# Kernel optimization log

Measured on AMD Instinct MI355X. Metric: run time of the kernel, lower is better.

## Reference

```python
import jax, jax.numpy as jnp
import numpy as np

B, T, D = 8, 512, 1024
H, DQK, DV = 16, 128, 128  # n_heads, d_qk = emb_dim//h_qk, d_v = emb_dim//h_v


def setup_inputs() -> dict:
    key = jax.random.key(0)
    ks = jax.random.split(key, 8)
    s = 0.02
    return {
        "X": jax.random.normal(ks[0], (B, T, D), jnp.float32),
        "pos_enc_k": jax.random.normal(ks[1], (T, T, DQK), jnp.float32) * s,
        "pos_enc_v": jax.random.normal(ks[2], (T, T, DV), jnp.float32) * s,
        "Wq": jax.random.normal(ks[3], (D, H * DQK), jnp.float32) * s,
        "bq": jnp.zeros((H * DQK,), jnp.float32),
        "Wk": jax.random.normal(ks[4], (D, H * DQK), jnp.float32) * s,
        "bk": jnp.zeros((H * DQK,), jnp.float32),
        "Wv": jax.random.normal(ks[5], (D, H * DV), jnp.float32) * s,
        "bv": jnp.zeros((H * DV,), jnp.float32),
        "Wp": jax.random.normal(ks[6], (H * DV, D), jnp.float32) * s,
        "bp": jnp.zeros((D,), jnp.float32),
    }


def reference(X, pos_enc_k, pos_enc_v, Wq, bq, Wk, bk, Wv, bv, Wp, bp):
    b, t, d = X.shape
    # projections -> (b, h, t, dhead)
    Q = (X @ Wq + bq).reshape(b, t, H, DQK).transpose(0, 2, 1, 3)
    K = (X @ Wk + bk).reshape(b, t, H, DQK).transpose(0, 2, 1, 3)
    V = (X @ Wv + bv).reshape(b, t, H, DV).transpose(0, 2, 1, 3)
    # content attention + relative-position key bias
    att = jnp.einsum("bhqd,bhkd->bhqk", Q, K)
    att = att + jnp.einsum("bhqd,qkd->bhqk", Q, pos_enc_k)
    att = att / jnp.sqrt(jnp.asarray(DQK, X.dtype))
    # causal mask (do_mask=True)
    causal = jnp.tril(jnp.ones((t, t), bool))
    att = jnp.where(causal[None, None], att, jnp.asarray(-jnp.inf, att.dtype))
    att = jax.nn.softmax(att, axis=-1)
    # values + relative-position value correction
    y = jnp.einsum("bhqk,bhkd->bhqd", att, V)
    y = y + jnp.einsum("bhqk,qkd->bhqd", att, pos_enc_v)
    y = y.transpose(0, 2, 1, 3).reshape(b, t, H * DV)
    return y @ Wp + bp
```

## Files before the change

kernel.cpp:

```cpp
#include <hip/hip_runtime.h>
#include <stdint.h>

#define B_  8
#define T_  512
#define D_  1024
#define H_  16
#define DH  128
#define BH  128
#define ND  2048
#define BT  4096

typedef __attribute__((ext_vector_type(8))) short          short8;
typedef __attribute__((ext_vector_type(8))) __bf16         bf16x8;
typedef __attribute__((ext_vector_type(4))) float          f32x4;
typedef __attribute__((ext_vector_type(4))) unsigned short ushort4v;

static __device__ __forceinline__ unsigned short f2bf(float f) {
  unsigned u = __builtin_bit_cast(unsigned, f);
  u += 0x7FFFu + ((u >> 16) & 1u);
  return (unsigned short)(u >> 16);
}
static __device__ __forceinline__ float bf2f(unsigned short h) {
  unsigned u = ((unsigned)h) << 16;
  return __builtin_bit_cast(float, u);
}
static __device__ __forceinline__ f32x4 mfma16(short8 a, short8 b, f32x4 c) {
  return __builtin_amdgcn_mfma_f32_16x16x32_bf16(
      __builtin_bit_cast(bf16x8, a), __builtin_bit_cast(bf16x8, b), c, 0, 0, 0);
}
static __device__ __forceinline__ void gload16(const unsigned short* g, unsigned short* l) {
  __builtin_amdgcn_global_load_lds(
      (const __attribute__((address_space(1))) void*)g,
      (__attribute__((address_space(3))) void*)l, 16, 0, 0);
}

template <int ROWS, int COLS>
static __device__ __forceinline__ void stage_gl2(unsigned short* lds,
                                                 const unsigned short* __restrict__ src,
                                                 long stride, int tid) {
  constexpr int CPR = COLS / 8;
#pragma unroll
  for (int it = 0; it < ROWS * COLS / 8 / 256; ++it) {
    int chunk = tid + it * 256;
    int r = chunk / CPR, c8 = (chunk % CPR) * 8;
    gload16(src + (long)r * stride + c8, lds + chunk * 8);
  }
}

template <int ROWS>
static __device__ __forceinline__ void stage_sw64(unsigned short* lds,
                                                  const unsigned short* __restrict__ src,
                                                  long stride, int tid) {
#pragma unroll
  for (int it = 0; it < ROWS / 32; ++it) {
    int n = tid + it * 256;
    int r = n >> 3, c = (n & 7) ^ (r & 7);
    gload16(src + (long)r * stride + c * 8, lds + n * 8);
  }
}

template <int MR, int NR, int LDA, int LDB, int KD>
static __device__ __forceinline__ void mfma_blk(const unsigned short* As,
                                                const unsigned short* Bs,
                                                int a0, int b0, int lrow, int lk8,
                                                f32x4 (*acc)[NR]) {
#pragma unroll
  for (int ks = 0; ks < KD; ks += 32) {
    short8 a[MR], b[NR];
#pragma unroll
    for (int i = 0; i < MR; ++i) a[i] = *(const short8*)&As[(a0 + i * 16 + lrow) * LDA + ks + lk8];
#pragma unroll
    for (int j = 0; j < NR; ++j) b[j] = *(const short8*)&Bs[(b0 + j * 16 + lrow) * LDB + ks + lk8];
#pragma unroll
    for (int i = 0; i < MR; ++i)
#pragma unroll
      for (int j = 0; j < NR; ++j) acc[i][j] = mfma16(a[i], b[j], acc[i][j]);
  }
}

template <int MR, int NR>
static __device__ __forceinline__ void mfma_sw64(const unsigned short* As,
                                                 const unsigned short* Bs,
                                                 int a0, int b0, int lrow, int g,
                                                 f32x4 (*acc)[NR]) {
#pragma unroll
  for (int ks = 0; ks < 2; ++ks) {
    short8 a[MR], b[NR];
#pragma unroll
    for (int i = 0; i < MR; ++i) {
      int ra = a0 + i * 16 + lrow;
      int c = (ks * 4 + g) ^ (ra & 7);
      a[i] = *(const short8*)&As[ra * 64 + c * 8];
    }
#pragma unroll
    for (int j = 0; j < NR; ++j) {
      int rb = b0 + j * 16 + lrow;
      int c = (ks * 4 + g) ^ (rb & 7);
      b[j] = *(const short8*)&Bs[rb * 64 + c * 8];
    }
#pragma unroll
    for (int i = 0; i < MR; ++i)
#pragma unroll
      for (int j = 0; j < NR; ++j) acc[i][j] = mfma16(a[i], b[j], acc[i][j]);
  }
}

#define IDS4                             \
  const int tid  = threadIdx.x;          \
  const int lane = tid & 63;             \
  const int wid  = tid >> 6;             \
  const int lrow = lane & 15;            \
  const int lk8  = (lane >> 4) * 8;      \
  const int lr4  = (lane >> 4) * 4;      \
  const int lg   = lane >> 4;            \
  const int wm = wid >> 1, wn = wid & 1;

#define LTS 132
#define LTQ 68

__global__ __launch_bounds__(256) void k_prep(const float* __restrict__ X,
                                              unsigned short* __restrict__ Xb,
                                              const float* __restrict__ Wq,
                                              const float* __restrict__ Wk,
                                              const float* __restrict__ Wv,
                                              const float* __restrict__ Wp,
                                              unsigned short* __restrict__ WT,
                                              unsigned short* __restrict__ WpT) {
  __shared__ float tile[32][33];
  int bid = blockIdx.x;
  if (bid < 4096) {
    int i = bid * 256 + threadIdx.x;
    f32x4 v = ((const f32x4*)X)[i];
    ushort4v o;
    o.x = f2bf(v.x); o.y = f2bf(v.y); o.z = f2bf(v.z); o.w = f2bf(v.w);
    ((ushort4v*)Xb)[i] = o;
    return;
  }
  bid -= 4096;
  const int which = bid >> 11;
  const int local = bid & 2047;
  const float* in;
  unsigned short* outp;
  int R, C, bx, by;
  if (which < 3) {
    in = which == 0 ? Wq : (which == 1 ? Wk : Wv);
    outp = WT + (size_t)which * ND * D_;
    R = D_; C = ND; bx = local & 63; by = local >> 6;
  } else {
    in = Wp; outp = WpT;
    R = ND; C = D_; bx = local & 31; by = local >> 5;
  }
  int c0 = bx * 32, r0 = by * 32;
  int tx = threadIdx.x & 31, ty = threadIdx.x >> 5;
#pragma unroll
  for (int i = 0; i < 32; i += 8)
    tile[ty + i][tx] = in[(long)(r0 + ty + i) * C + (c0 + tx)];
  __syncthreads();
#pragma unroll
  for (int i = 0; i < 32; i += 8)
    outp[(long)(c0 + ty + i) * R + (r0 + tx)] = f2bf(tile[tx][ty + i]);
}

__global__ __launch_bounds__(256) void k_vtrans(const unsigned short* __restrict__ vin,
                                                unsigned short* __restrict__ vout) {
  __shared__ unsigned short tile[32][33];
  int bh = blockIdx.z;
  int t0 = blockIdx.x * 32, d0 = blockIdx.y * 32;
  int tx = threadIdx.x & 31, ty = threadIdx.x >> 5;
#pragma unroll
  for (int i = 0; i < 32; i += 8)
    tile[ty + i][tx] = vin[((long)bh * T_ + t0 + ty + i) * DH + (d0 + tx)];
  __syncthreads();
#pragma unroll
  for (int i = 0; i < 32; i += 8)
    vout[((long)bh * DH + (d0 + ty + i)) * T_ + (t0 + tx)] = tile[tx][ty + i];
}

__global__ __launch_bounds__(256) void k_proj8(const unsigned short* __restrict__ Xb,
                                               const unsigned short* __restrict__ WT,
                                               const float* __restrict__ bq,
                                               const float* __restrict__ bk,
                                               const float* __restrict__ bv,
                                               unsigned short* __restrict__ Qb,
                                               unsigned short* __restrict__ Kb,
                                               unsigned short* __restrict__ Vb) {
  __shared__ unsigned short As[128 * 64], Bs[128 * 64];
  IDS4
  const int flat = blockIdx.x, xcd = flat & 7, local = flat >> 3;
  const int nt = xcd * 6 + (local % 6);
  const int mt = local / 6;
  const int m0 = mt * 128, n0 = nt * 128;

  f32x4 acc[4][4] = {};
  for (int kk = 0; kk < D_; kk += 64) {
    stage_gl2<128, 64>(As, Xb + (long)m0 * D_ + kk, D_, tid);
    stage_gl2<128, 64>(Bs, WT + (long)n0 * D_ + kk, D_, tid);
    __syncthreads();
    mfma_blk<4, 4, 64, 64, 64>(As, Bs, wm * 64, wn * 64, lrow, lk8, acc);
    __syncthreads();
  }

  const int nb = n0 >> 11;
  const float* biasp = nb == 0 ? bq : (nb == 1 ? bk : bv);
  unsigned short* dst = nb == 0 ? Qb : (nb == 1 ? Kb : Vb);
  const int hcol = (n0 & 2047) >> 7;
#pragma unroll
  for (int i = 0; i < 4; ++i)
#pragma unroll
    for (int j = 0; j < 4; ++j) {
      int cc = (n0 & 2047) + wn * 64 + j * 16 + lrow;
      int dd = cc & 127;
      float bias = biasp[cc];
#pragma unroll
      for (int r = 0; r < 4; ++r) {
        int m = m0 + wm * 64 + i * 16 + lr4 + r;
        int bb = m >> 9, tt = m & (T_ - 1);
        dst[((long)(bb * H_ + hcol) * T_ + tt) * DH + dd] = f2bf(acc[i][j][r] + bias);
      }
    }
}

__global__ __launch_bounds__(256) void k_posk(const unsigned short* __restrict__ Qb,
                                              const float* __restrict__ Pk,
                                              unsigned short* __restrict__ att) {
  const int bid = blockIdx.x;
  const int q = (bid & 1) ? (T_ - 1 - (bid >> 1)) : (bid >> 1);
  const int ktiles = (q >> 6) + 1;
  __shared__ unsigned short As[128 * 128];
  __shared__ unsigned short Bs[2][64 * 136];
  IDS4
  {
    const unsigned short* src = Qb + (long)q * DH;
#pragma unroll
    for (int it = 0; it < 8; ++it) {
      int n = tid + it * 256;
      int r = n >> 4, c = (n & 15) ^ (r & 7);
      gload16(src + (long)r * (T_ * DH) + c * 8, As + n * 8);
    }
  }
  f32x4 pv[8];
  const float* psrc = Pk + (long)q * T_ * DH;
  auto loadPk = [&](int kt) {
#pragma unroll
    for (int it = 0; it < 8; ++it) {
      int chunk = tid + it * 256;
      int r = chunk >> 5, c4 = (chunk & 31) * 4;
      pv[it] = *(const f32x4*)(psrc + (long)(kt * 64 + r) * DH + c4);
    }
  };
  auto writeB = [&](int buf) {
#pragma unroll
    for (int it = 0; it < 8; ++it) {
      int chunk = tid + it * 256;
      int r = chunk >> 5, c4 = (chunk & 31) * 4;
      ushort4v o;
      o.x = f2bf(pv[it].x); o.y = f2bf(pv[it].y); o.z = f2bf(pv[it].z); o.w = f2bf(pv[it].w);
      *(ushort4v*)&Bs[buf][r * 136 + c4] = o;
    }
  };
  loadPk(0);
  asm volatile("s_waitcnt vmcnt(0)" ::: "memory");
  writeB(0);
  asm volatile("s_waitcnt lgkmcnt(0)" ::: "memory");
  __builtin_amdgcn_s_barrier();
  for (int kt = 0; kt < ktiles; ++kt) {
    const bool pre = (kt + 1 < ktiles);
    if (pre) loadPk(kt + 1);
    f32x4 acc[4][2] = {};
#pragma unroll
    for (int ks = 0; ks < 4; ++ks) {
      short8 a[4], b[2];
#pragma unroll
      for (int i = 0; i < 4; ++i) {
        int ra = wm * 64 + i * 16 + lrow;
        int c = (ks * 4 + lg) ^ (ra & 7);
        a[i] = *(const short8*)&As[ra * 128 + c * 8];
      }
#pragma unroll
      for (int j = 0; j < 2; ++j)
        b[j] = *(const short8*)&Bs[kt & 1][(wn * 32 + j * 16 + lrow) * 136 + ks * 32 + lk8];
#pragma unroll
      for (int i = 0; i < 4; ++i)
#pragma unroll
        for (int j = 0; j < 2; ++j)
          acc[i][j] = mfma16(a[i], b[j], acc[i][j]);
    }
    if (pre) {
      asm volatile("s_waitcnt vmcnt(0)" ::: "memory");
      writeB((kt + 1) & 1);
    }
#pragma unroll
    for (int i = 0; i < 4; ++i)
#pragma unroll
      for (int j = 0; j < 2; ++j) {
        int k = kt * 64 + wn * 32 + j * 16 + lrow;
#pragma unroll
        for (int r = 0; r < 4; ++r) {
          int bh = wm * 64 + i * 16 + lr4 + r;
          att[((long)q * BH + bh) * T_ + k] = f2bf(acc[i][j][r]);
        }
      }
    asm volatile("s_waitcnt lgkmcnt(0)" ::: "memory");
    __builtin_amdgcn_s_barrier();
  }
}

__global__ __launch_bounds__(256) void k_qkv(const unsigned short* __restrict__ Qb,
                                             const unsigned short* __restrict__ Kb,
                                             const unsigned short* __restrict__ Vt,
                                             unsigned short* __restrict__ att,
                                             float* __restrict__ Sinv,
                                             unsigned short* __restrict__ Ybb) {
  const int bh = blockIdx.x & 127, pr = blockIdx.x >> 7;
  __shared__ unsigned short Qs[64 * 128], Ks[64 * 128], Vs[128 * 64];
  __shared__ unsigned short Ps[64 * 72];
  __shared__ float lt[64 * LTQ];
  __shared__ float sInv[64];
  const int tid = threadIdx.x;
  const int lane = tid & 63, wid = tid >> 6;
  const int wm = wid >> 1, wn = wid & 1;
  const int lrow = lane & 15, lk8 = (lane >> 4) * 8, lr4 = (lane >> 4) * 4;
  const int row = tid >> 2, c0 = (tid & 3) * 16;
  const float scale = 0.08838834764831845f;
  const int b = bh >> 4, h = bh & 15;

  for (int pass = 0; pass < 2; ++pass) {
    const int qt = pass ? 7 - pr : pr;
    const int q0 = qt * 64, ktiles = qt + 1;
    const int qabs = q0 + row;
    unsigned short* arow = att + ((long)qabs * BH + bh) * T_;
    {
      const unsigned short* src = Qb + ((long)bh * T_ + q0) * DH;
#pragma unroll
      for (int it = 0; it < 4; ++it) {
        int n = tid + it * 256;
        int r = n >> 4, c = (n & 15) ^ (r & 7);
        gload16(src + (long)r * DH + c * 8, Qs + n * 8);
      }
    }
    float ssum = 0.f;
    f32x4 accv[2][4] = {};
    for (int kt = 0; kt < ktiles; ++kt) {
      const unsigned short* ksrc = Kb + ((long)bh * T_ + kt * 64) * DH;
#pragma unroll
      for (int it = 0; it < 4; ++it) {
        int n = tid + it * 256;
        int r = n >> 4, c = (n & 15) ^ (r & 7);
        gload16(ksrc + (long)r * DH + c * 8, Ks + n * 8);
      }
      const unsigned short* vsrc = Vt + (long)bh * DH * T_ + kt * 64;
#pragma unroll
      for (int it = 0; it < 4; ++it) {
        int n = tid + it * 256;
        int r = n >> 3, c = (n & 7) ^ (r & 7);
        gload16(vsrc + (long)r * T_ + c * 8, Vs + n * 8);
      }
      short8 pb0 = *(const short8*)(arow + kt * 64 + c0);
      short8 pb1 = *(const short8*)(arow + kt * 64 + c0 + 8);
      __syncthreads();
      f32x4 acc[2][2] = {};
#pragma unroll
      for (int ks = 0; ks < 4; ++ks) {
        short8 aq[2], bk2[2];
#pragma unroll
        for (int i = 0; i < 2; ++i) {
          int ra = wm * 32 + i * 16 + lrow;
          int c = (ks * 4 + (lane >> 4)) ^ (ra & 7);
          aq[i] = *(const short8*)&Qs[ra * 128 + c * 8];
        }
#pragma unroll
        for (int j = 0; j < 2; ++j) {
          int rb = wn * 32 + j * 16 + lrow;
          int c = (ks * 4 + (lane >> 4)) ^ (rb & 7);
          bk2[j] = *(const short8*)&Ks[rb * 128 + c * 8];
        }
#pragma unroll
        for (int i = 0; i < 2; ++i)
#pragma unroll
          for (int j = 0; j < 2; ++j)
            acc[i][j] = mfma16(aq[i], bk2[j], acc[i][j]);
      }
#pragma unroll
      for (int i = 0; i < 2; ++i)
#pragma unroll
        for (int j = 0; j < 2; ++j)
#pragma unroll
          for (int r = 0; r < 4; ++r)
            lt[(wm * 32 + i * 16 + lr4 + r) * LTQ + wn * 32 + j * 16 + lrow] = acc[i][j][r];
      __syncthreads();
      short8 o0, o1;
#pragma unroll
      for (int jj = 0; jj < 8; ++jj) {
        int k = kt * 64 + c0 + jj;
        float e0 = (k <= qabs)
                   ? __expf((lt[row * LTQ + c0 + jj] + bf2f((unsigned short)pb0[jj])) * scale) : 0.f;
        float e1 = (k + 8 <= qabs)
                   ? __expf((lt[row * LTQ + c0 + 8 + jj] + bf2f((unsigned short)pb1[jj])) * scale) : 0.f;
        o0[jj] = (short)f2bf(e0);
        o1[jj] = (short)f2bf(e1);
        ssum += e0 + e1;
      }
      *(short8*)(arow + kt * 64 + c0) = o0;
      *(short8*)(arow + kt * 64 + c0 + 8) = o1;
      *(short8*)&Ps[row * 72 + c0] = o0;
      *(short8*)&Ps[row * 72 + c0 + 8] = o1;
      __syncthreads();
#pragma unroll
      for (int ks = 0; ks < 2; ++ks) {
        short8 ap[2], bv2[4];
#pragma unroll
        for (int i = 0; i < 2; ++i) {
          int ra = wm * 32 + i * 16 + lrow;
          ap[i] = *(const short8*)&Ps[ra * 72 + ks * 32 + lk8];
        }
#pragma unroll
        for (int j = 0; j < 4; ++j) {
          int rb = wn * 64 + j * 16 + lrow;
          int c = ((ks * 4) + (lane >> 4)) ^ (rb & 7);
          bv2[j] = *(const short8*)&Vs[rb * 64 + c * 8];
        }
#pragma unroll
        for (int i = 0; i < 2; ++i)
#pragma unroll
          for (int j = 0; j < 4; ++j)
            accv[i][j] = mfma16(ap[i], bv2[j], accv[i][j]);
      }
      __syncthreads();
    }
    ssum += __shfl_xor(ssum, 1, 64);
    ssum += __shfl_xor(ssum, 2, 64);
    float si = 1.f / ssum;
    if ((tid & 3) == 0) { sInv[row] = si; Sinv[(long)qabs * BH + bh] = si; }
    __syncthreads();
#pragma unroll
    for (int i = 0; i < 2; ++i) {
      float sc2[4];
#pragma unroll
      for (int r = 0; r < 4; ++r) sc2[r] = sInv[wm * 32 + i * 16 + lr4 + r];
#pragma unroll
      for (int j = 0; j < 4; ++j) {
        int d = wn * 64 + j * 16 + lrow;
#pragma unroll
        for (int r = 0; r < 4; ++r) {
          int q = q0 + wm * 32 + i * 16 + lr4 + r;
          Ybb[(long)(b * T_ + q) * ND + h * DH + d] = f2bf(accv[i][j][r] * sc2[r]);
        }
      }
    }
    __syncthreads();
  }
}

__global__ __launch_bounds__(256) void k_posv(const unsigned short* __restrict__ P,
                                              const float* __restrict__ Pv,
                                              const float* __restrict__ Sinv,
                                              unsigned short* __restrict__ Ybb) {
  const int bid = blockIdx.x;
  const int q = (bid & 1) ? (T_ - 1 - (bid >> 1)) : (bid >> 1);
  const int ktiles = (q >> 6) + 1;
  __shared__ unsigned short As[128 * 64];
  __shared__ unsigned short Bs[2][128 * 72];
  __shared__ float lt[64 * LTQ];
  IDS4
  f32x4 pv[8];
  const float* psrc = Pv + (long)q * T_ * DH;
  auto loadPv = [&](int kt) {
#pragma unroll
    for (int it = 0; it < 8; ++it) {
      int chunk = tid + it * 256;
      int d4 = (chunk & 3) * 4 + ((chunk >> 6) & 7) * 16;
      int k  = ((chunk >> 2) & 15) + ((chunk >> 9) & 3) * 16;
      pv[it] = *(const f32x4*)(psrc + (long)(kt * 64 + k) * DH + d4);
    }
  };
  auto writeB = [&](int buf) {
#pragma unroll
    for (int it = 0; it < 8; ++it) {
      int chunk = tid + it * 256;
      int d4 = (chunk & 3) * 4 + ((chunk >> 6) & 7) * 16;
      int k  = ((chunk >> 2) & 15) + ((chunk >> 9) & 3) * 16;
      Bs[buf][(d4 + 0) * 72 + k] = f2bf(pv[it].x);
      Bs[buf][(d4 + 1) * 72 + k] = f2bf(pv[it].y);
      Bs[buf][(d4 + 2) * 72 + k] = f2bf(pv[it].z);
      Bs[buf][(d4 + 3) * 72 + k] = f2bf(pv[it].w);
    }
  };
  loadPv(0);
  asm volatile("s_waitcnt vmcnt(0)" ::: "memory");
  writeB(0);
  asm volatile("s_waitcnt lgkmcnt(0)" ::: "memory");
  __builtin_amdgcn_s_barrier();
  f32x4 acc[4][4] = {};
  for (int kt = 0; kt < ktiles; ++kt) {
    const bool pre = (kt + 1 < ktiles);
    stage_sw64<128>(As, P + (long)q * BH * T_ + kt * 64, T_, tid);
    if (pre) loadPv(kt + 1);
    if (pre) asm volatile("s_waitcnt vmcnt(8)" ::: "memory");
    else     asm volatile("s_waitcnt vmcnt(0)" ::: "memory");
    __builtin_amdgcn_s_barrier();
#pragma unroll
    for (int ks = 0; ks < 2; ++ks) {
      short8 a[4], b[4];
#pragma unroll
      for (int i = 0; i < 4; ++i) {
        int ra = wm * 64 + i * 16 + lrow;
        int c = (ks * 4 + lg) ^ (ra & 7);
        a[i] = *(const short8*)&As[ra * 64 + c * 8];
      }
#pragma unroll
      for (int j = 0; j < 4; ++j)
        b[j] = *(const short8*)&Bs[kt & 1][(wn * 64 + j * 16 + lrow) * 72 + ks * 32 + lk8];
#pragma unroll
      for (int i = 0; i < 4; ++i)
#pragma unroll
        for (int j = 0; j < 4; ++j)
          acc[i][j] = mfma16(a[i], b[j], acc[i][j]);
    }
    if (pre) {
      asm volatile("s_waitcnt vmcnt(0)" ::: "memory");
      writeB((kt + 1) & 1);
    }
    asm volatile("s_waitcnt lgkmcnt(0)" ::: "memory");
    __builtin_amdgcn_s_barrier();
  }
  const int row = tid >> 2, c0 = (tid & 3) * 16;
#pragma unroll
  for (int hb = 0; hb < 2; ++hb)
#pragma unroll
    for (int hd = 0; hd < 2; ++hd) {
      int bh = hb * 64 + row;
      long idx = ((long)((bh >> 4) * T_ + q)) * ND + (bh & 15) * DH + hd * 64 + c0;
      short8 y0 = *(const short8*)&Ybb[idx];
      short8 y1 = *(const short8*)&Ybb[idx + 8];
      float sc = Sinv[(long)q * BH + bh];
      if (wm == hb && wn == hd) {
#pragma unroll
        for (int i = 0; i < 4; ++i)
#pragma unroll
          for (int j = 0; j < 4; ++j)
#pragma unroll
            for (int r = 0; r < 4; ++r)
              lt[(i * 16 + lr4 + r) * LTQ + j * 16 + lrow] = acc[i][j][r];
      }
      __syncthreads();
      short8 o0, o1;
#pragma unroll
      for (int jj = 0; jj < 8; ++jj) {
        o0[jj] = (short)f2bf(lt[row * LTQ + c0 + jj] * sc + bf2f((unsigned short)y0[jj]));
        o1[jj] = (short)f2bf(lt[row * LTQ + c0 + 8 + jj] * sc + bf2f((unsigned short)y1[jj]));
      }
      *(short8*)&Ybb[idx] = o0;
      *(short8*)&Ybb[idx + 8] = o1;
      __syncthreads();
    }
}

__global__ __launch_bounds__(256) void k_oproj(const unsigned short* __restrict__ Ybb,
                                               const unsigned short* __restrict__ WpT,
                                               const float* __restrict__ bp,
                                               float* __restrict__ outp) {
  __shared__ unsigned short As[128 * 64], Bs[128 * 64];
  IDS4
  const int m0 = blockIdx.y * 128, n0 = blockIdx.x * 128;
  f32x4 acc[4][4] = {};
  for (int kk = 0; kk < ND; kk += 64) {
    stage_sw64<128>(As, Ybb + (long)m0 * ND + kk, ND, tid);
    stage_sw64<128>(Bs, WpT + (long)n0 * ND + kk, ND, tid);
    __syncthreads();
    mfma_sw64<4, 4>(As, Bs, wm * 64, wn * 64, lrow, lg, acc);
    __syncthreads();
  }
  float* lt = (float*)As;
  const int row = tid >> 4, c8 = (tid & 15) * 8;
  f32x4 b0 = *(const f32x4*)(bp + n0 + c8);
  f32x4 b1 = *(const f32x4*)(bp + n0 + c8 + 4);
#pragma unroll
  for (int rr = 0; rr < 8; ++rr) {
    if (wm == (rr >> 2)) {
      const int ii = rr & 3;
#pragma unroll
      for (int j = 0; j < 4; ++j)
#pragma unroll
        for (int r = 0; r < 4; ++r)
          lt[(lr4 + r) * LTS + wn * 64 + j * 16 + lrow] = acc[ii][j][r];
    }
    __syncthreads();
    f32x4 v0 = *(const f32x4*)&lt[row * LTS + c8];
    f32x4 v1 = *(const f32x4*)&lt[row * LTS + c8 + 4];
    int m = m0 + rr * 16 + row;
    v0.x += b0.x; v0.y += b0.y; v0.z += b0.z; v0.w += b0.w;
    v1.x += b1.x; v1.y += b1.y; v1.z += b1.z; v1.w += b1.w;
    *(f32x4*)&outp[(long)m * D_ + n0 + c8] = v0;
    *(f32x4*)&outp[(long)m * D_ + n0 + c8 + 4] = v1;
    __syncthreads();
  }
}

extern "C" void kernel_launch(void* const* d_in, const int* in_sizes, int n_in,
                              void* d_out, int out_size, void* d_ws, size_t ws_size,
                              hipStream_t stream) {
  const float* X  = (const float*)d_in[0];
  const float* Pk = (const float*)d_in[1];
  const float* Pv = (const float*)d_in[2];
  const float* Wq = (const float*)d_in[3];
  const float* bq = (const float*)d_in[4];
  const float* Wk = (const float*)d_in[5];
  const float* bk = (const float*)d_in[6];
  const float* Wv = (const float*)d_in[7];
  const float* bv = (const float*)d_in[8];
  const float* Wp = (const float*)d_in[9];
  const float* bp = (const float*)d_in[10];
  float* out = (float*)d_out;

  uint8_t* w = (uint8_t*)d_ws;
  unsigned short* Xb  = (unsigned short*)w; w += (size_t)BT * D_ * 2;
  unsigned short* WT  = (unsigned short*)w; w += (size_t)3 * ND * D_ * 2;
  unsigned short* WpT = (unsigned short*)w; w += (size_t)D_ * ND * 2;
  unsigned short* Qb  = (unsigned short*)w; w += (size_t)BH * T_ * DH * 2;
  unsigned short* Kb  = (unsigned short*)w; w += (size_t)BH * T_ * DH * 2;
  unsigned short* Vb  = (unsigned short*)w; w += (size_t)BH * T_ * DH * 2;
  unsigned short* Vt  = (unsigned short*)w; w += (size_t)BH * DH * T_ * 2;
  unsigned short* att = (unsigned short*)w; w += (size_t)T_ * BH * T_ * 2;
  unsigned short* Ybb = (unsigned short*)w; w += (size_t)BT * ND * 2;
  float*          Sinv= (float*)w;          w += (size_t)T_ * BH * 4;

  k_prep<<<12288, 256, 0, stream>>>(X, Xb, Wq, Wk, Wv, Wp, WT, WpT);
  k_proj8<<<1536, 256, 0, stream>>>(Xb, WT, bq, bk, bv, Qb, Kb, Vb);
  k_vtrans<<<dim3(T_ / 32, DH / 32, BH), 256, 0, stream>>>(Vb, Vt);
  k_posk<<<T_, 256, 0, stream>>>(Qb, Pk, att);
  k_qkv<<<512, 256, 0, stream>>>(Qb, Kb, Vt, att, Sinv, Ybb);
  k_posv<<<T_, 256, 0, stream>>>(att, Pv, Sinv, Ybb);
  k_oproj<<<dim3(D_ / 128, BT / 128), 256, 0, stream>>>(Ybb, WpT, bp, out);
}
```

Before: 255.6 us.

## Fuse V transpose into projection epilogue and use swizzled LDS staging

The projection GEMM now writes V directly in transposed (d-major) layout, which removes the separate k_vtrans kernel and its extra round trip of V through global memory. The GEMM main loop also switches from plain LDS staging to the XOR-swizzled 64-column staging and MFMA reads, to cut LDS bank conflicts. The transposed epilogue stores are strided along t, so write coalescing for the V blocks may be worse.

```diff
diff --git a/kernel.cpp b/kernel.cpp
--- a/kernel.cpp
+++ b/kernel.cpp
@@ -56,25 +56,6 @@
     int n = tid + it * 256;
     int r = n >> 3, c = (n & 7) ^ (r & 7);
     gload16(src + (long)r * stride + c * 8, lds + n * 8);
-  }
-}
-
-template <int MR, int NR, int LDA, int LDB, int KD>
-static __device__ __forceinline__ void mfma_blk(const unsigned short* As,
-                                                const unsigned short* Bs,
-                                                int a0, int b0, int lrow, int lk8,
-                                                f32x4 (*acc)[NR]) {
-#pragma unroll
-  for (int ks = 0; ks < KD; ks += 32) {
-    short8 a[MR], b[NR];
-#pragma unroll
-    for (int i = 0; i < MR; ++i) a[i] = *(const short8*)&As[(a0 + i * 16 + lrow) * LDA + ks + lk8];
-#pragma unroll
-    for (int j = 0; j < NR; ++j) b[j] = *(const short8*)&Bs[(b0 + j * 16 + lrow) * LDB + ks + lk8];
-#pragma unroll
-    for (int i = 0; i < MR; ++i)
-#pragma unroll
-      for (int j = 0; j < NR; ++j) acc[i][j] = mfma16(a[i], b[j], acc[i][j]);
   }
 }
 
@@ -161,21 +142,6 @@
     outp[(long)(c0 + ty + i) * R + (r0 + tx)] = f2bf(tile[tx][ty + i]);
 }
 
-__global__ __launch_bounds__(256) void k_vtrans(const unsigned short* __restrict__ vin,
-                                                unsigned short* __restrict__ vout) {
-  __shared__ unsigned short tile[32][33];
-  int bh = blockIdx.z;
-  int t0 = blockIdx.x * 32, d0 = blockIdx.y * 32;
-  int tx = threadIdx.x & 31, ty = threadIdx.x >> 5;
-#pragma unroll
-  for (int i = 0; i < 32; i += 8)
-    tile[ty + i][tx] = vin[((long)bh * T_ + t0 + ty + i) * DH + (d0 + tx)];
-  __syncthreads();
-#pragma unroll
-  for (int i = 0; i < 32; i += 8)
-    vout[((long)bh * DH + (d0 + ty + i)) * T_ + (t0 + tx)] = tile[tx][ty + i];
-}
-
 __global__ __launch_bounds__(256) void k_proj8(const unsigned short* __restrict__ Xb,
                                                const unsigned short* __restrict__ WT,
                                                const float* __restrict__ bq,
@@ -183,7 +149,7 @@
                                                const float* __restrict__ bv,
                                                unsigned short* __restrict__ Qb,
                                                unsigned short* __restrict__ Kb,
-                                               unsigned short* __restrict__ Vb) {
+                                               unsigned short* __restrict__ Vt) {
   __shared__ unsigned short As[128 * 64], Bs[128 * 64];
   IDS4
   const int flat = blockIdx.x, xcd = flat & 7, local = flat >> 3;
@@ -193,31 +159,48 @@
 
   f32x4 acc[4][4] = {};
   for (int kk = 0; kk < D_; kk += 64) {
-    stage_gl2<128, 64>(As, Xb + (long)m0 * D_ + kk, D_, tid);
-    stage_gl2<128, 64>(Bs, WT + (long)n0 * D_ + kk, D_, tid);
-    __syncthreads();
-    mfma_blk<4, 4, 64, 64, 64>(As, Bs, wm * 64, wn * 64, lrow, lk8, acc);
+    stage_sw64<128>(As, Xb + (long)m0 * D_ + kk, D_, tid);
+    stage_sw64<128>(Bs, WT + (long)n0 * D_ + kk, D_, tid);
+    __syncthreads();
+    mfma_sw64<4, 4>(As, Bs, wm * 64, wn * 64, lrow, lg, acc);
     __syncthreads();
   }
 
   const int nb = n0 >> 11;
   const float* biasp = nb == 0 ? bq : (nb == 1 ? bk : bv);
-  unsigned short* dst = nb == 0 ? Qb : (nb == 1 ? Kb : Vb);
   const int hcol = (n0 & 2047) >> 7;
-#pragma unroll
-  for (int i = 0; i < 4; ++i)
-#pragma unroll
-    for (int j = 0; j < 4; ++j) {
-      int cc = (n0 & 2047) + wn * 64 + j * 16 + lrow;
-      int dd = cc & 127;
-      float bias = biasp[cc];
-#pragma unroll
-      for (int r = 0; r < 4; ++r) {
-        int m = m0 + wm * 64 + i * 16 + lr4 + r;
-        int bb = m >> 9, tt = m & (T_ - 1);
-        dst[((long)(bb * H_ + hcol) * T_ + tt) * DH + dd] = f2bf(acc[i][j][r] + bias);
-      }
-    }
+  if (nb < 2) {
+    unsigned short* dst = nb == 0 ? Qb : Kb;
+#pragma unroll
+    for (int i = 0; i < 4; ++i)
+#pragma unroll
+      for (int j = 0; j < 4; ++j) {
+        int cc = (n0 & 2047) + wn * 64 + j * 16 + lrow;
+        int dd = cc & 127;
+        float bias = biasp[cc];
+#pragma unroll
+        for (int r = 0; r < 4; ++r) {
+          int m = m0 + wm * 64 + i * 16 + lr4 + r;
+          int bb = m >> 9, tt = m & (T_ - 1);
+          dst[((long)(bb * H_ + hcol) * T_ + tt) * DH + dd] = f2bf(acc[i][j][r] + bias);
+        }
+      }
+  } else {
+#pragma unroll
+    for (int i = 0; i < 4; ++i)
+#pragma unroll
+      for (int j = 0; j < 4; ++j) {
+        int cc = (n0 & 2047) + wn * 64 + j * 16 + lrow;
+        int dd = cc & 127;
+        float bias = biasp[cc];
+#pragma unroll
+        for (int r = 0; r < 4; ++r) {
+          int m = m0 + wm * 64 + i * 16 + lr4 + r;
+          int bb = m >> 9, tt = m & (T_ - 1);
+          Vt[((long)(bb * H_ + hcol) * DH + dd) * T_ + tt] = f2bf(acc[i][j][r] + bias);
+        }
+      }
+  }
 }
 
 __global__ __launch_bounds__(256) void k_posk(const unsigned short* __restrict__ Qb,
@@ -618,15 +601,13 @@
   unsigned short* WpT = (unsigned short*)w; w += (size_t)D_ * ND * 2;
   unsigned short* Qb  = (unsigned short*)w; w += (size_t)BH * T_ * DH * 2;
   unsigned short* Kb  = (unsigned short*)w; w += (size_t)BH * T_ * DH * 2;
-  unsigned short* Vb  = (unsigned short*)w; w += (size_t)BH * T_ * DH * 2;
   unsigned short* Vt  = (unsigned short*)w; w += (size_t)BH * DH * T_ * 2;
   unsigned short* att = (unsigned short*)w; w += (size_t)T_ * BH * T_ * 2;
   unsigned short* Ybb = (unsigned short*)w; w += (size_t)BT * ND * 2;
   float*          Sinv= (float*)w;          w += (size_t)T_ * BH * 4;
 
   k_prep<<<12288, 256, 0, stream>>>(X, Xb, Wq, Wk, Wv, Wp, WT, WpT);
-  k_proj8<<<1536, 256, 0, stream>>>(Xb, WT, bq, bk, bv, Qb, Kb, Vb);
-  k_vtrans<<<dim3(T_ / 32, DH / 32, BH), 256, 0, stream>>>(Vb, Vt);
+  k_proj8<<<1536, 256, 0, stream>>>(Xb, WT, bq, bk, bv, Qb, Kb, Vt);
   k_posk<<<T_, 256, 0, stream>>>(Qb, Pk, att);
   k_qkv<<<512, 256, 0, stream>>>(Qb, Kb, Vt, att, Sinv, Ybb);
   k_posv<<<T_, 256, 0, stream>>>(att, Pv, Sinv, Ybb);
```

Measured after the change: 238.4 us. 1.07x faster.
